# Kernel optimization log

Measured on AMD Instinct MI355X. Metric: run time of the kernel, lower is better.

Reference implementation:

```python
import jax, jax.numpy as jnp
import numpy as np

EPS = 1e-5
GROUPS = 8


def setup_inputs() -> dict:
    key = jax.random.key(0)
    ks = jax.random.split(key, 3)
    b, c, h, w = 8, 256, 64, 64
    x = jax.random.normal(ks[0], (b, c, h, w), dtype=jnp.float32)
    # 1x1 convs are just channel matmuls; store weights as [out_ch, in_ch]
    qkv_w = jax.random.normal(ks[1], (3 * c, c), dtype=jnp.float32) * (c ** -0.5)
    qkv_b = jnp.zeros((3 * c,), dtype=jnp.float32)
    out_w = jax.random.normal(ks[2], (c, c), dtype=jnp.float32) * (c ** -0.5)
    out_b = jnp.zeros((c,), dtype=jnp.float32)
    gn_w = jnp.ones((c,), dtype=jnp.float32)
    gn_b = jnp.zeros((c,), dtype=jnp.float32)
    return {"x": x, "gn_w": gn_w, "gn_b": gn_b, "qkv_w": qkv_w,
            "qkv_b": qkv_b, "out_w": out_w, "out_b": out_b}


def _group_norm(x, gn_w, gn_b):
    # x: [b, c, h, w]; normalize per (group, sample) over (c//g, h, w)
    b, c, h, w = x.shape
    xg = x.reshape(b, GROUPS, c // GROUPS, h * w)
    mean = xg.mean(axis=(2, 3), keepdims=True)
    var = xg.var(axis=(2, 3), keepdims=True)
    xn = (xg - mean) * jax.lax.rsqrt(var + EPS)
    xn = xn.reshape(b, c, h * w)
    return xn * gn_w[None, :, None] + gn_b[None, :, None]


def reference(x, gn_w, gn_b, qkv_w, qkv_b, out_w, out_b):
    b, c, h, w = x.shape
    scale = 1.0 / np.sqrt(c).astype(np.float32)  # matches channels ** -0.5
    nx = _group_norm(x, gn_w, gn_b)                       # [b, c, n]
    qkv = jnp.einsum('oc,bcn->bon', qkv_w, nx) + qkv_b[None, :, None]
    q, k, v = qkv[:, :c], qkv[:, c:2 * c], qkv[:, 2 * c:]  # each [b, c, n]
    attn = jnp.einsum('bci,bcj->bij', q, k) * scale        # [b, n, n]
    attn = jax.nn.softmax(attn, axis=-1)
    out = jnp.einsum('bij,bcj->bci', attn, v)              # [b, c, n]
    out = jnp.einsum('oc,bcn->bon', out_w, out) + out_b[None, :, None]
    return out.reshape(b, c, h, w) + x
```

## Files before the change

### kernel.cpp

```cpp
#include <hip/hip_runtime.h>
#include <math.h>


#define Bn 8
#define Cn 256
#define HWn 4096
#define Gn 8
#define CPGn 32
#define Mqkv 768
#define EPSf 1e-5f
#define QSCALEf 0.0625f
#define RTHR 8.0f

typedef short bf16x8 __attribute__((ext_vector_type(8)));
typedef float f32x4 __attribute__((ext_vector_type(4)));

__device__ __forceinline__ unsigned short f2bf(float f) {
  union { float f; unsigned u; } v; v.f = f;
  unsigned r = v.u + 0x7FFFu + ((v.u >> 16) & 1u);
  return (unsigned short)(r >> 16);
}

__device__ __forceinline__ int cvt_pk_bf16(float lo, float hi) {
  int d;
  asm("v_cvt_pk_bf16_f32 %0, %1, %2" : "=v"(d) : "v"(lo), "v"(hi));
  return d;
}

__global__ __launch_bounds__(1024)
void gn_stats_kernel(const float* __restrict__ x, const float* __restrict__ gn_w,
                     const float* __restrict__ gn_b, float* __restrict__ s_out,
                     float* __restrict__ t_out) {
  const int b = blockIdx.x / Gn, g = blockIdx.x % Gn;
  const float4* base = (const float4*)(x + ((size_t)(b * Cn + g * CPGn)) * HWn);
  const int n4 = CPGn * HWn / 4;
  float sum = 0.f, sq = 0.f;
  for (int i = threadIdx.x; i < n4; i += 1024) {
    float4 v = base[i];
    sum += (v.x + v.y) + (v.z + v.w);
    sq  += (v.x * v.x + v.y * v.y) + (v.z * v.z + v.w * v.w);
  }
  __shared__ float ss[1024], s2[1024];
  ss[threadIdx.x] = sum; s2[threadIdx.x] = sq;
  __syncthreads();
  for (int off = 512; off > 0; off >>= 1) {
    if ((int)threadIdx.x < off) {
      ss[threadIdx.x] += ss[threadIdx.x + off];
      s2[threadIdx.x] += s2[threadIdx.x + off];
    }
    __syncthreads();
  }
  if (threadIdx.x < CPGn) {
    const float inv_n = 1.f / (float)(CPGn * HWn);
    float mean = ss[0] * inv_n;
    float var  = s2[0] * inv_n - mean * mean;
    float rstd = rsqrtf(var + EPSf);
    int c = g * CPGn + (int)threadIdx.x;
    float sc = gn_w[c] * rstd;
    s_out[b * Cn + c] = sc;
    t_out[b * Cn + c] = gn_b[c] - mean * sc;
  }
}

__global__ __launch_bounds__(256)
void affine_transpose_kernel(const float* __restrict__ x, const float* __restrict__ s_aff,
                             const float* __restrict__ t_aff, unsigned short* __restrict__ nxT) {
  const int bid = blockIdx.x;
  const int b = bid & 7, r = bid >> 3;
  const int c0 = (r & 3) * 64, n0 = (r >> 2) * 64;
  const int tid = threadIdx.x;
  __shared__ unsigned int ld32[64][33];
  const float* xb = x + ((size_t)(b * Cn + c0)) * HWn + n0;
  const int cl0 = tid >> 4, nn = (tid & 15) * 4;
#pragma unroll
  for (int it = 0; it < 4; ++it) {
    int cl = cl0 + 16 * it;
    int c = c0 + cl;
    float sc = s_aff[b * Cn + c], sh = t_aff[b * Cn + c];
    float4 v = *(const float4*)(xb + (size_t)cl * HWn + nn);
    ld32[cl][(nn >> 1) + 0] = (unsigned)cvt_pk_bf16(v.x * sc + sh, v.y * sc + sh);
    ld32[cl][(nn >> 1) + 1] = (unsigned)cvt_pk_bf16(v.z * sc + sh, v.w * sc + sh);
  }
  __syncthreads();
#pragma unroll
  for (int it = 0; it < 2; ++it) {
    int chunk = tid + 256 * it;
    int n = chunk >> 3, cg = chunk & 7;
    union { unsigned short u[8]; bf16x8 v; } o;
#pragma unroll
    for (int k = 0; k < 8; ++k) {
      unsigned w32 = ld32[cg * 8 + k][n >> 1];
      o.u[k] = (unsigned short)((n & 1) ? (w32 >> 16) : (w32 & 0xffffu));
    }
    *(bf16x8*)(nxT + ((size_t)(b * HWn + n0 + n)) * Cn + c0 + cg * 8) = o.v;
  }
}

__global__ __launch_bounds__(256, 2)
void qkv_gemm_kernel(const unsigned short* __restrict__ nxT, const float* __restrict__ w,
                     const float* __restrict__ wb, unsigned short* __restrict__ Qt,
                     unsigned short* __restrict__ Kt, unsigned short* __restrict__ Vb) {
  const int bid = blockIdx.x;
  const int b = bid & 7, r = bid >> 3;
  const int n0 = (r & 63) * 64, m0 = (r >> 6) * 128;
  const int tid = threadIdx.x;
  const int wv = tid >> 6, l = tid & 63;
  const int l15 = l & 15, lq = l >> 4;
  const int ob = m0 + wv * 32;

  bf16x8 wf[2][8];
#pragma unroll
  for (int g = 0; g < 2; ++g) {
    const float* wr = w + (size_t)(ob + g * 16 + l15) * Cn + lq * 8;
#pragma unroll
    for (int kc = 0; kc < 8; ++kc) {
      float4 a = *(const float4*)(wr + kc * 32);
      float4 c4 = *(const float4*)(wr + kc * 32 + 4);
      union { int w4[4]; bf16x8 v; } u;
      u.w4[0] = cvt_pk_bf16(a.x, a.y);  u.w4[1] = cvt_pk_bf16(a.z, a.w);
      u.w4[2] = cvt_pk_bf16(c4.x, c4.y); u.w4[3] = cvt_pk_bf16(c4.z, c4.w);
      wf[g][kc] = u.v;
    }
  }

  const unsigned short* nb = nxT + (size_t)b * HWn * Cn + lq * 8;
  f32x4 acc[2][4];
#pragma unroll
  for (int g = 0; g < 2; ++g)
#pragma unroll
    for (int s = 0; s < 4; ++s) acc[g][s] = (f32x4)(0.f);

  const bool isV = (m0 >= 512);
#pragma unroll
  for (int s = 0; s < 4; ++s) {
    const unsigned short* np = nb + (size_t)(n0 + s * 16 + l15) * Cn;
#pragma unroll
    for (int kc = 0; kc < 8; ++kc) {
      bf16x8 xf = *(const bf16x8*)(np + kc * 32);
      if (!isV) {
        acc[0][s] = __builtin_amdgcn_mfma_f32_16x16x32_bf16(wf[0][kc], xf, acc[0][s], 0, 0, 0);
        acc[1][s] = __builtin_amdgcn_mfma_f32_16x16x32_bf16(wf[1][kc], xf, acc[1][s], 0, 0, 0);
      } else {
        acc[0][s] = __builtin_amdgcn_mfma_f32_16x16x32_bf16(xf, wf[0][kc], acc[0][s], 0, 0, 0);
        acc[1][s] = __builtin_amdgcn_mfma_f32_16x16x32_bf16(xf, wf[1][kc], acc[1][s], 0, 0, 0);
      }
    }
  }

  if (!isV) {
    unsigned short* dst = (m0 < 256) ? Qt : Kt;
    const float scl = (m0 < 256) ? QSCALEf : 1.0f;
#pragma unroll
    for (int g = 0; g < 2; ++g) {
      int cb = ((ob + g * 16) & 255) + lq * 4;
      float b0 = wb[ob + g * 16 + lq * 4 + 0];
      float b1 = wb[ob + g * 16 + lq * 4 + 1];
      float b2 = wb[ob + g * 16 + lq * 4 + 2];
      float b3 = wb[ob + g * 16 + lq * 4 + 3];
#pragma unroll
      for (int s = 0; s < 4; ++s) {
        int n = n0 + s * 16 + l15;
        ushort4 pk;
        pk.x = f2bf((acc[g][s][0] + b0) * scl);
        pk.y = f2bf((acc[g][s][1] + b1) * scl);
        pk.z = f2bf((acc[g][s][2] + b2) * scl);
        pk.w = f2bf((acc[g][s][3] + b3) * scl);
        *(ushort4*)(dst + ((size_t)(b * HWn + n)) * Cn + cb) = pk;
      }
    }
  } else {
#pragma unroll
    for (int g = 0; g < 2; ++g) {
      int o = ob + g * 16 + l15;
      int c = o - 512;
      float bias = wb[o];
#pragma unroll
      for (int s = 0; s < 4; ++s) {
        int n = n0 + s * 16 + lq * 4;
        ushort4 pk;
        pk.x = f2bf(acc[g][s][0] + bias);
        pk.y = f2bf(acc[g][s][1] + bias);
        pk.z = f2bf(acc[g][s][2] + bias);
        pk.w = f2bf(acc[g][s][3] + bias);
        *(ushort4*)(Vb + ((size_t)(b * Cn + c)) * HWn + n) = pk;
      }
    }
  }
}

__global__ __launch_bounds__(256, 2)
void attn_kernel(const unsigned short* __restrict__ Qt,
                 const unsigned short* __restrict__ Kt,
                 const unsigned short* __restrict__ Vb,
                 unsigned short* __restrict__ outp) {
  const int bid = blockIdx.x;
  const int b = bid & 7, i0 = (bid >> 3) * 64;
  const int tid = threadIdx.x;
  const int wv = tid >> 6, l = tid & 63;
  const int l15 = l & 15, lq = l >> 4;

  __shared__ unsigned short Ks[8192];
  __shared__ unsigned short Vs[8192];
  char* KsB = (char*)Ks;
  char* VsB = (char*)Vs;

  const unsigned short* Qb = Qt + ((size_t)b * HWn + i0) * Cn;
  const unsigned short* Kb = Kt + (size_t)b * HWn * Cn;
  const unsigned short* Vg = Vb + (size_t)b * Cn * HWn;

  bf16x8 qf[8];
  {
    const unsigned short* qrow = Qb + (size_t)(wv * 16 + l15) * Cn + lq * 8;
#pragma unroll
    for (int kc = 0; kc < 8; ++kc) qf[kc] = *(const bf16x8*)(qrow + kc * 32);
  }

  const int jk = ((tid >> 6) & 1) * 16 + (tid & 15);
  const int ck = (tid >> 7) * 32 + ((tid >> 4) & 3) * 8;
  const int cv = (tid >> 6) * 16 + (tid & 15);
  const int jv = ((tid >> 4) & 3) * 8;
  const unsigned short* gK = Kb + (size_t)jk * Cn + ck;
  const unsigned short* gV = Vg + (size_t)cv * HWn + jv;

  const int laneA = l15 + ((lq & 1) << 5);
  const int laneB = laneA + 16;
  const int shi = lq >> 1;

  bf16x8 kst[4], vst[4];
#pragma unroll
  for (int q = 0; q < 4; ++q) kst[q] = *(const bf16x8*)(gK + q * 64);
#pragma unroll
  for (int q = 0; q < 4; ++q) vst[q] = *(const bf16x8*)(gV + (size_t)q * 64 * HWn);
  gK += 32 * Cn; gV += 32;

  f32x4 o_acc[16];
#pragma unroll
  for (int cs = 0; cs < 16; ++cs) o_acc[cs] = (f32x4)(0.f);
  float m_i = -INFINITY, l_i = 0.f;

#pragma unroll 1
  for (int t = 0; t < 128; ++t) {
#pragma unroll
    for (int q = 0; q < 4; ++q) *(bf16x8*)(KsB + tid * 16 + q * 4096) = kst[q];
#pragma unroll
    for (int q = 0; q < 4; ++q) *(bf16x8*)(VsB + tid * 16 + q * 4096) = vst[q];
    __syncthreads();
    if (t < 127) {
#pragma unroll
      for (int q = 0; q < 4; ++q) kst[q] = *(const bf16x8*)(gK + q * 64);
#pragma unroll
      for (int q = 0; q < 4; ++q) vst[q] = *(const bf16x8*)(gV + (size_t)q * 64 * HWn);
      gK += 32 * Cn; gV += 32;
    }

    f32x4 s0 = (f32x4)(0.f), s1 = (f32x4)(0.f);
#pragma unroll
    for (int kc = 0; kc < 8; ++kc) {
      bf16x8 kf0 = *(const bf16x8*)(KsB + l * 16 + kc * 2048);
      bf16x8 kf1 = *(const bf16x8*)(KsB + l * 16 + kc * 2048 + 1024);
      s0 = __builtin_amdgcn_mfma_f32_16x16x32_bf16(kf0, qf[kc], s0, 0, 0, 0);
      s1 = __builtin_amdgcn_mfma_f32_16x16x32_bf16(kf1, qf[kc], s1, 0, 0, 0);
    }

    float p[2][4];
#pragma unroll
    for (int u = 0; u < 4; ++u) { p[0][u] = s0[u]; p[1][u] = s1[u]; }
    float rm = fmaxf(fmaxf(fmaxf(p[0][0], p[0][1]), fmaxf(p[0][2], p[0][3])),
                     fmaxf(fmaxf(p[1][0], p[1][1]), fmaxf(p[1][2], p[1][3])));
    rm = fmaxf(rm, __shfl_xor(rm, 16));
    rm = fmaxf(rm, __shfl_xor(rm, 32));
    if (!__all(rm - m_i <= RTHR)) {
      float mn = fmaxf(m_i, rm);
      float alpha = __expf(m_i - mn);
      m_i = mn;
      l_i *= alpha;
      float a0 = __shfl(alpha, 4 * lq + 0);
      float a1 = __shfl(alpha, 4 * lq + 1);
      float a2 = __shfl(alpha, 4 * lq + 2);
      float a3 = __shfl(alpha, 4 * lq + 3);
#pragma unroll
      for (int cs = 0; cs < 16; ++cs) {
        o_acc[cs][0] *= a0; o_acc[cs][1] *= a1;
        o_acc[cs][2] *= a2; o_acc[cs][3] *= a3;
      }
    }
    float rs = 0.f;
#pragma unroll
    for (int s = 0; s < 2; ++s)
#pragma unroll
      for (int u = 0; u < 4; ++u) { float e = __expf(p[s][u] - m_i); p[s][u] = e; rs += e; }
    rs += __shfl_xor(rs, 16);
    rs += __shfl_xor(rs, 32);
    l_i += rs;

    int d00 = cvt_pk_bf16(p[0][0], p[0][1]), d01 = cvt_pk_bf16(p[0][2], p[0][3]);
    int d10 = cvt_pk_bf16(p[1][0], p[1][1]), d11 = cvt_pk_bf16(p[1][2], p[1][3]);
    int A00 = __shfl(d00, laneA), A01 = __shfl(d01, laneA);
    int A10 = __shfl(d10, laneA), A11 = __shfl(d11, laneA);
    int B00 = __shfl(d00, laneB), B01 = __shfl(d01, laneB);
    int B10 = __shfl(d10, laneB), B11 = __shfl(d11, laneB);
    union { int w[4]; bf16x8 v; } pa;
    pa.w[0] = shi ? A10 : A00; pa.w[1] = shi ? A11 : A01;
    pa.w[2] = shi ? B10 : B00; pa.w[3] = shi ? B11 : B01;

#pragma unroll
    for (int cs = 0; cs < 16; ++cs) {
      bf16x8 vf = *(const bf16x8*)(VsB + l * 16 + cs * 1024);
      o_acc[cs] = __builtin_amdgcn_mfma_f32_16x16x32_bf16(pa.v, vf, o_acc[cs], 0, 0, 0);
    }
    __syncthreads();
  }

  float il = 1.f / l_i;
  float i0v = __shfl(il, 4 * lq + 0);
  float i1v = __shfl(il, 4 * lq + 1);
  float i2v = __shfl(il, 4 * lq + 2);
  float i3v = __shfl(il, 4 * lq + 3);
  unsigned short* ob = outp + (size_t)b * HWn * Cn;
  const int ibase = i0 + wv * 16 + lq * 4;
#pragma unroll
  for (int cs = 0; cs < 16; ++cs) {
    int c = cs * 16 + l15;
    ob[(size_t)(ibase + 0) * Cn + c] = f2bf(o_acc[cs][0] * i0v);
    ob[(size_t)(ibase + 1) * Cn + c] = f2bf(o_acc[cs][1] * i1v);
    ob[(size_t)(ibase + 2) * Cn + c] = f2bf(o_acc[cs][2] * i2v);
    ob[(size_t)(ibase + 3) * Cn + c] = f2bf(o_acc[cs][3] * i3v);
  }
}

__global__ __launch_bounds__(256, 2)
void out_gemm_kernel(const unsigned short* __restrict__ tmpT, const float* __restrict__ w,
                     const float* __restrict__ wb, const float* __restrict__ xres,
                     float* __restrict__ y) {
  const int bid = blockIdx.x;
  const int b = bid & 7, r = bid >> 3;
  const int n0 = (r & 63) * 64, m0 = (r >> 6) * 128;
  const int tid = threadIdx.x;
  const int wv = tid >> 6, l = tid & 63;
  const int l15 = l & 15, lq = l >> 4;
  const int ob = m0 + wv * 32;

  bf16x8 wf[2][8];
#pragma unroll
  for (int g = 0; g < 2; ++g) {
    const float* wr = w + (size_t)(ob + g * 16 + l15) * Cn + lq * 8;
#pragma unroll
    for (int kc = 0; kc < 8; ++kc) {
      float4 a = *(const float4*)(wr + kc * 32);
      float4 c4 = *(const float4*)(wr + kc * 32 + 4);
      union { int w4[4]; bf16x8 v; } u;
      u.w4[0] = cvt_pk_bf16(a.x, a.y);  u.w4[1] = cvt_pk_bf16(a.z, a.w);
      u.w4[2] = cvt_pk_bf16(c4.x, c4.y); u.w4[3] = cvt_pk_bf16(c4.z, c4.w);
      wf[g][kc] = u.v;
    }
  }

  const unsigned short* tb = tmpT + (size_t)b * HWn * Cn + lq * 8;
  f32x4 acc[2][4];
#pragma unroll
  for (int g = 0; g < 2; ++g)
#pragma unroll
    for (int s = 0; s < 4; ++s) acc[g][s] = (f32x4)(0.f);

#pragma unroll
  for (int s = 0; s < 4; ++s) {
    const unsigned short* tp = tb + (size_t)(n0 + s * 16 + l15) * Cn;
#pragma unroll
    for (int kc = 0; kc < 8; ++kc) {
      bf16x8 tf = *(const bf16x8*)(tp + kc * 32);
      acc[0][s] = __builtin_amdgcn_mfma_f32_16x16x32_bf16(tf, wf[0][kc], acc[0][s], 0, 0, 0);
      acc[1][s] = __builtin_amdgcn_mfma_f32_16x16x32_bf16(tf, wf[1][kc], acc[1][s], 0, 0, 0);
    }
  }

#pragma unroll
  for (int g = 0; g < 2; ++g) {
    int o = ob + g * 16 + l15;
    float bias = wb[o];
#pragma unroll
    for (int s = 0; s < 4; ++s) {
      int n = n0 + s * 16 + lq * 4;
      size_t idx = ((size_t)(b * Cn + o)) * HWn + n;
      float4 xr = *(const float4*)(xres + idx);
      float4 out;
      out.x = acc[g][s][0] + bias + xr.x;
      out.y = acc[g][s][1] + bias + xr.y;
      out.z = acc[g][s][2] + bias + xr.z;
      out.w = acc[g][s][3] + bias + xr.w;
      *(float4*)(y + idx) = out;
    }
  }
}

extern "C" void kernel_launch(void* const* d_in, const int* in_sizes, int n_in,
                              void* d_out, int out_size, void* d_ws, size_t ws_size,
                              hipStream_t stream) {
  (void)in_sizes; (void)n_in; (void)out_size; (void)ws_size;
  const float* x     = (const float*)d_in[0];
  const float* gn_w  = (const float*)d_in[1];
  const float* gn_b  = (const float*)d_in[2];
  const float* qkv_w = (const float*)d_in[3];
  const float* qkv_b = (const float*)d_in[4];
  const float* out_w = (const float*)d_in[5];
  const float* out_b = (const float*)d_in[6];
  float* out = (float*)d_out;

  char* ws = (char*)d_ws;
  float* s_aff = (float*)ws;
  float* t_aff = s_aff + Bn * Cn;
  unsigned short* Qt  = (unsigned short*)(ws + 16384);
  unsigned short* Kt  = Qt  + (size_t)Bn * HWn * Cn;
  unsigned short* Vb  = Kt  + (size_t)Bn * HWn * Cn;
  unsigned short* nxT = Vb  + (size_t)Bn * HWn * Cn;
  unsigned short* tmpT = nxT + (size_t)Bn * HWn * Cn;

  gn_stats_kernel<<<dim3(Bn * Gn), 1024, 0, stream>>>(x, gn_w, gn_b, s_aff, t_aff);
  affine_transpose_kernel<<<dim3(2048), 256, 0, stream>>>(x, s_aff, t_aff, nxT);
  qkv_gemm_kernel<<<dim3(3072), 256, 0, stream>>>(nxT, qkv_w, qkv_b, Qt, Kt, Vb);
  attn_kernel<<<dim3(512), 256, 0, stream>>>(Qt, Kt, Vb, tmpT);
  out_gemm_kernel<<<dim3(1024), 256, 0, stream>>>(tmpT, out_w, out_b, x, out);
}
```

Measured before the change: 397.2 us.

## Split attention over key dimension into four partitions with combine kernel

Splits each attention query tile's key/value range into four partitions, launching four times as many blocks, each writing unnormalized bf16 partial outputs plus running max and sum. A new combine kernel merges the partials with log-sum-exp weights, and the output GEMM reads the combined tile layout. This aims to raise parallelism and improve load balance across CUs, at the cost of extra partial-output memory traffic, an extra launch, and repeated Q loads.

```diff
diff --git a/kernel.cpp b/kernel.cpp
--- a/kernel.cpp
+++ b/kernel.cpp
@@ -19,6 +19,11 @@
   union { float f; unsigned u; } v; v.f = f;
   unsigned r = v.u + 0x7FFFu + ((v.u >> 16) & 1u);
   return (unsigned short)(r >> 16);
+}
+
+__device__ __forceinline__ float bf2f(unsigned short u) {
+  union { unsigned u; float f; } v; v.u = ((unsigned)u) << 16;
+  return v.f;
 }
 
 __device__ __forceinline__ int cvt_pk_bf16(float lo, float hi) {
@@ -192,9 +197,9 @@
 void attn_kernel(const unsigned short* __restrict__ Qt,
                  const unsigned short* __restrict__ Kt,
                  const unsigned short* __restrict__ Vb,
-                 unsigned short* __restrict__ outp) {
+                 unsigned short* __restrict__ pO, float* __restrict__ pML) {
   const int bid = blockIdx.x;
-  const int b = bid & 7, i0 = (bid >> 3) * 64;
+  const int b = bid & 7, part = (bid >> 3) & 3, i0 = (bid >> 5) * 64;
   const int tid = threadIdx.x;
   const int wv = tid >> 6, l = tid & 63;
   const int l15 = l & 15, lq = l >> 4;
@@ -219,8 +224,8 @@
   const int ck = (tid >> 7) * 32 + ((tid >> 4) & 3) * 8;
   const int cv = (tid >> 6) * 16 + (tid & 15);
   const int jv = ((tid >> 4) & 3) * 8;
-  const unsigned short* gK = Kb + (size_t)jk * Cn + ck;
-  const unsigned short* gV = Vg + (size_t)cv * HWn + jv;
+  const unsigned short* gK = Kb + (size_t)(jk + part * 1024) * Cn + ck;
+  const unsigned short* gV = Vg + (size_t)cv * HWn + jv + part * 1024;
 
   const int laneA = l15 + ((lq & 1) << 5);
   const int laneB = laneA + 16;
@@ -239,13 +244,13 @@
   float m_i = -INFINITY, l_i = 0.f;
 
 #pragma unroll 1
-  for (int t = 0; t < 128; ++t) {
+  for (int t = 0; t < 32; ++t) {
 #pragma unroll
     for (int q = 0; q < 4; ++q) *(bf16x8*)(KsB + tid * 16 + q * 4096) = kst[q];
 #pragma unroll
     for (int q = 0; q < 4; ++q) *(bf16x8*)(VsB + tid * 16 + q * 4096) = vst[q];
     __syncthreads();
-    if (t < 127) {
+    if (t < 31) {
 #pragma unroll
       for (int q = 0; q < 4; ++q) kst[q] = *(const bf16x8*)(gK + q * 64);
 #pragma unroll
@@ -311,25 +316,72 @@
     __syncthreads();
   }
 
-  float il = 1.f / l_i;
-  float i0v = __shfl(il, 4 * lq + 0);
-  float i1v = __shfl(il, 4 * lq + 1);
-  float i2v = __shfl(il, 4 * lq + 2);
-  float i3v = __shfl(il, 4 * lq + 3);
-  unsigned short* ob = outp + (size_t)b * HWn * Cn;
-  const int ibase = i0 + wv * 16 + lq * 4;
+  unsigned short* pOb = pO + (size_t)bid * (64 * 256);
+  const int ibase = wv * 16 + lq * 4;
 #pragma unroll
   for (int cs = 0; cs < 16; ++cs) {
     int c = cs * 16 + l15;
-    ob[(size_t)(ibase + 0) * Cn + c] = f2bf(o_acc[cs][0] * i0v);
-    ob[(size_t)(ibase + 1) * Cn + c] = f2bf(o_acc[cs][1] * i1v);
-    ob[(size_t)(ibase + 2) * Cn + c] = f2bf(o_acc[cs][2] * i2v);
-    ob[(size_t)(ibase + 3) * Cn + c] = f2bf(o_acc[cs][3] * i3v);
+    pOb[(ibase + 0) * 256 + c] = f2bf(o_acc[cs][0]);
+    pOb[(ibase + 1) * 256 + c] = f2bf(o_acc[cs][1]);
+    pOb[(ibase + 2) * 256 + c] = f2bf(o_acc[cs][2]);
+    pOb[(ibase + 3) * 256 + c] = f2bf(o_acc[cs][3]);
+  }
+  if (lq == 0) {
+    pML[(size_t)bid * 128 + (wv * 16 + l15) * 2 + 0] = m_i;
+    pML[(size_t)bid * 128 + (wv * 16 + l15) * 2 + 1] = l_i;
+  }
+}
+
+__global__ __launch_bounds__(256)
+void attn_combine_kernel(unsigned short* __restrict__ pO, const float* __restrict__ pML) {
+  const int bid = blockIdx.x;
+  const int b = bid & 7, itile = bid >> 3;
+  const int tid = threadIdx.x;
+  const int p0id = b + (itile << 5);
+  unsigned short* B0 = pO + (size_t)p0id * (64 * 256);
+  const unsigned short* B1 = pO + (size_t)(p0id + 8)  * (64 * 256);
+  const unsigned short* B2 = pO + (size_t)(p0id + 16) * (64 * 256);
+  const unsigned short* B3 = pO + (size_t)(p0id + 24) * (64 * 256);
+
+  __shared__ float gS[4][64];
+  if (tid < 64) {
+    float m0v = pML[(size_t)p0id * 128 + tid * 2],        l0v = pML[(size_t)p0id * 128 + tid * 2 + 1];
+    float m1v = pML[(size_t)(p0id + 8) * 128 + tid * 2],  l1v = pML[(size_t)(p0id + 8) * 128 + tid * 2 + 1];
+    float m2v = pML[(size_t)(p0id + 16) * 128 + tid * 2], l2v = pML[(size_t)(p0id + 16) * 128 + tid * 2 + 1];
+    float m3v = pML[(size_t)(p0id + 24) * 128 + tid * 2], l3v = pML[(size_t)(p0id + 24) * 128 + tid * 2 + 1];
+    float ms = fmaxf(fmaxf(m0v, m1v), fmaxf(m2v, m3v));
+    float w0 = __expf(m0v - ms), w1 = __expf(m1v - ms);
+    float w2 = __expf(m2v - ms), w3 = __expf(m3v - ms);
+    float den = w0 * l0v + w1 * l1v + w2 * l2v + w3 * l3v;
+    float id = 1.f / den;
+    gS[0][tid] = w0 * id; gS[1][tid] = w1 * id;
+    gS[2][tid] = w2 * id; gS[3][tid] = w3 * id;
+  }
+  __syncthreads();
+
+#pragma unroll
+  for (int k = 0; k < 8; ++k) {
+    int chunk = tid + 256 * k;
+    int row = chunk >> 5, cc = (chunk & 31) * 8;
+    int off = row * 256 + cc;
+    float g0 = gS[0][row], g1 = gS[1][row], g2 = gS[2][row], g3 = gS[3][row];
+    union { unsigned short u[8]; bf16x8 v; } v0, v1, v2, v3, o;
+    v0.v = *(const bf16x8*)(B0 + off);
+    v1.v = *(const bf16x8*)(B1 + off);
+    v2.v = *(const bf16x8*)(B2 + off);
+    v3.v = *(const bf16x8*)(B3 + off);
+#pragma unroll
+    for (int e = 0; e < 8; ++e) {
+      float val = g0 * bf2f(v0.u[e]) + g1 * bf2f(v1.u[e]) +
+                  g2 * bf2f(v2.u[e]) + g3 * bf2f(v3.u[e]);
+      o.u[e] = f2bf(val);
+    }
+    *(bf16x8*)(B0 + off) = o.v;
   }
 }
 
 __global__ __launch_bounds__(256, 2)
-void out_gemm_kernel(const unsigned short* __restrict__ tmpT, const float* __restrict__ w,
+void out_gemm_kernel(const unsigned short* __restrict__ pO, const float* __restrict__ w,
                      const float* __restrict__ wb, const float* __restrict__ xres,
                      float* __restrict__ y) {
   const int bid = blockIdx.x;
@@ -355,7 +407,7 @@
     }
   }
 
-  const unsigned short* tb = tmpT + (size_t)b * HWn * Cn + lq * 8;
+  const unsigned short* tb = pO + ((size_t)(b + ((n0 >> 6) << 5)) * (64 * 256)) + lq * 8;
   f32x4 acc[2][4];
 #pragma unroll
   for (int g = 0; g < 2; ++g)
@@ -364,7 +416,7 @@
 
 #pragma unroll
   for (int s = 0; s < 4; ++s) {
-    const unsigned short* tp = tb + (size_t)(n0 + s * 16 + l15) * Cn;
+    const unsigned short* tp = tb + (size_t)(s * 16 + l15) * Cn;
 #pragma unroll
     for (int kc = 0; kc < 8; ++kc) {
       bf16x8 tf = *(const bf16x8*)(tp + kc * 32);
@@ -406,17 +458,20 @@
   float* out = (float*)d_out;
 
   char* ws = (char*)d_ws;
+  const size_t BHC = (size_t)Bn * HWn * Cn;
   float* s_aff = (float*)ws;
   float* t_aff = s_aff + Bn * Cn;
   unsigned short* Qt  = (unsigned short*)(ws + 16384);
-  unsigned short* Kt  = Qt  + (size_t)Bn * HWn * Cn;
-  unsigned short* Vb  = Kt  + (size_t)Bn * HWn * Cn;
-  unsigned short* nxT = Vb  + (size_t)Bn * HWn * Cn;
-  unsigned short* tmpT = nxT + (size_t)Bn * HWn * Cn;
+  unsigned short* Kt  = Qt + BHC;
+  unsigned short* Vb  = Kt + BHC;
+  unsigned short* nxT = Vb + BHC;
+  unsigned short* pO  = nxT;
+  float* pML = (float*)((char*)pO + (size_t)2048 * 16384 * 2);
 
   gn_stats_kernel<<<dim3(Bn * Gn), 1024, 0, stream>>>(x, gn_w, gn_b, s_aff, t_aff);
   affine_transpose_kernel<<<dim3(2048), 256, 0, stream>>>(x, s_aff, t_aff, nxT);
   qkv_gemm_kernel<<<dim3(3072), 256, 0, stream>>>(nxT, qkv_w, qkv_b, Qt, Kt, Vb);
-  attn_kernel<<<dim3(512), 256, 0, stream>>>(Qt, Kt, Vb, tmpT);
-  out_gemm_kernel<<<dim3(1024), 256, 0, stream>>>(tmpT, out_w, out_b, x, out);
-}
+  attn_kernel<<<dim3(2048), 256, 0, stream>>>(Qt, Kt, Vb, pO, pML);
+  attn_combine_kernel<<<dim3(512), 256, 0, stream>>>(pO, pML);
+  out_gemm_kernel<<<dim3(1024), 256, 0, stream>>>(pO, out_w, out_b, x, out);
+}
```

Result: slower. 424.5 us (+6.9%).

## Switch attention kernel to 32x32x16 MFMA with split query/channel wave tiling

Applied to the files above, without the earlier changes.

The flash-attention kernel moves from 16x16x32 to 32x32x16 bf16 MFMA. Waves now tile as 2 query groups of 32 rows by 2 channel halves, where before each of the 4 waves owned 16 query rows. The K/V staging layouts and the P fragment exchange change to match: a single xor-32 shuffle replaces the laneA/laneB gathers, and the per-row alpha and 1/l broadcast shuffles go away. Final stores become vectorized ushort4 writes. The aim is fewer LDS reads per FLOP and less shuffle overhead. In exchange, the QK^T product is computed twice, once per channel-half wave, which adds redundant MFMA work.

```diff
diff --git a/kernel.cpp b/kernel.cpp
--- a/kernel.cpp
+++ b/kernel.cpp
@@ -14,6 +14,7 @@
 
 typedef short bf16x8 __attribute__((ext_vector_type(8)));
 typedef float f32x4 __attribute__((ext_vector_type(4)));
+typedef float f32x16 __attribute__((ext_vector_type(16)));
 
 __device__ __forceinline__ unsigned short f2bf(float f) {
   union { float f; unsigned u; } v; v.f = f;
@@ -197,7 +198,8 @@
   const int b = bid & 7, i0 = (bid >> 3) * 64;
   const int tid = threadIdx.x;
   const int wv = tid >> 6, l = tid & 63;
-  const int l15 = l & 15, lq = l >> 4;
+  const int l31 = l & 31, hi = l >> 5;
+  const int rg = wv >> 1, cw = wv & 1;
 
   __shared__ unsigned short Ks[8192];
   __shared__ unsigned short Vs[8192];
@@ -208,23 +210,16 @@
   const unsigned short* Kb = Kt + (size_t)b * HWn * Cn;
   const unsigned short* Vg = Vb + (size_t)b * Cn * HWn;
 
-  bf16x8 qf[8];
+  bf16x8 qf[16];
   {
-    const unsigned short* qrow = Qb + (size_t)(wv * 16 + l15) * Cn + lq * 8;
-#pragma unroll
-    for (int kc = 0; kc < 8; ++kc) qf[kc] = *(const bf16x8*)(qrow + kc * 32);
-  }
-
-  const int jk = ((tid >> 6) & 1) * 16 + (tid & 15);
-  const int ck = (tid >> 7) * 32 + ((tid >> 4) & 3) * 8;
-  const int cv = (tid >> 6) * 16 + (tid & 15);
-  const int jv = ((tid >> 4) & 3) * 8;
-  const unsigned short* gK = Kb + (size_t)jk * Cn + ck;
-  const unsigned short* gV = Vg + (size_t)cv * HWn + jv;
-
-  const int laneA = l15 + ((lq & 1) << 5);
-  const int laneB = laneA + 16;
-  const int shi = lq >> 1;
+    const unsigned short* qrow = Qb + (size_t)(rg * 32 + l31) * Cn + hi * 8;
+#pragma unroll
+    for (int kc = 0; kc < 16; ++kc) qf[kc] = *(const bf16x8*)(qrow + kc * 16);
+  }
+
+  const unsigned short* gK = Kb + (size_t)(tid & 31) * Cn + (tid >> 5) * 8;
+  const unsigned short* gV = Vg + (size_t)((tid >> 7) * 32 + (tid & 31)) * HWn
+                                + ((tid >> 5) & 3) * 8;
 
   bf16x8 kst[4], vst[4];
 #pragma unroll
@@ -233,10 +228,10 @@
   for (int q = 0; q < 4; ++q) vst[q] = *(const bf16x8*)(gV + (size_t)q * 64 * HWn);
   gK += 32 * Cn; gV += 32;
 
-  f32x4 o_acc[16];
-#pragma unroll
-  for (int cs = 0; cs < 16; ++cs) o_acc[cs] = (f32x4)(0.f);
+  f32x16 o0 = (f32x16)(0.f), o1 = (f32x16)(0.f);
+  f32x16 o2 = (f32x16)(0.f), o3 = (f32x16)(0.f);
   float m_i = -INFINITY, l_i = 0.f;
+  const int vbase = cw * 4 * 2048;
 
 #pragma unroll 1
   for (int t = 0; t < 128; ++t) {
@@ -253,78 +248,89 @@
       gK += 32 * Cn; gV += 32;
     }
 
-    f32x4 s0 = (f32x4)(0.f), s1 = (f32x4)(0.f);
-#pragma unroll
-    for (int kc = 0; kc < 8; ++kc) {
-      bf16x8 kf0 = *(const bf16x8*)(KsB + l * 16 + kc * 2048);
-      bf16x8 kf1 = *(const bf16x8*)(KsB + l * 16 + kc * 2048 + 1024);
-      s0 = __builtin_amdgcn_mfma_f32_16x16x32_bf16(kf0, qf[kc], s0, 0, 0, 0);
-      s1 = __builtin_amdgcn_mfma_f32_16x16x32_bf16(kf1, qf[kc], s1, 0, 0, 0);
-    }
-
-    float p[2][4];
-#pragma unroll
-    for (int u = 0; u < 4; ++u) { p[0][u] = s0[u]; p[1][u] = s1[u]; }
-    float rm = fmaxf(fmaxf(fmaxf(p[0][0], p[0][1]), fmaxf(p[0][2], p[0][3])),
-                     fmaxf(fmaxf(p[1][0], p[1][1]), fmaxf(p[1][2], p[1][3])));
-    rm = fmaxf(rm, __shfl_xor(rm, 16));
+    f32x16 sa = (f32x16)(0.f);
+#pragma unroll
+    for (int kc = 0; kc < 16; ++kc) {
+      bf16x8 kf = *(const bf16x8*)(KsB + l * 16 + kc * 1024);
+      sa = __builtin_amdgcn_mfma_f32_32x32x16_bf16(kf, qf[kc], sa, 0, 0, 0);
+    }
+
+    float p[16];
+#pragma unroll
+    for (int r = 0; r < 16; ++r) p[r] = sa[r];
+    float rm = p[0];
+#pragma unroll
+    for (int r = 1; r < 16; ++r) rm = fmaxf(rm, p[r]);
     rm = fmaxf(rm, __shfl_xor(rm, 32));
     if (!__all(rm - m_i <= RTHR)) {
       float mn = fmaxf(m_i, rm);
       float alpha = __expf(m_i - mn);
       m_i = mn;
       l_i *= alpha;
-      float a0 = __shfl(alpha, 4 * lq + 0);
-      float a1 = __shfl(alpha, 4 * lq + 1);
-      float a2 = __shfl(alpha, 4 * lq + 2);
-      float a3 = __shfl(alpha, 4 * lq + 3);
-#pragma unroll
-      for (int cs = 0; cs < 16; ++cs) {
-        o_acc[cs][0] *= a0; o_acc[cs][1] *= a1;
-        o_acc[cs][2] *= a2; o_acc[cs][3] *= a3;
+#pragma unroll
+      for (int r = 0; r < 16; ++r) {
+        o0[r] *= alpha; o1[r] *= alpha; o2[r] *= alpha; o3[r] *= alpha;
       }
     }
     float rs = 0.f;
 #pragma unroll
-    for (int s = 0; s < 2; ++s)
-#pragma unroll
-      for (int u = 0; u < 4; ++u) { float e = __expf(p[s][u] - m_i); p[s][u] = e; rs += e; }
-    rs += __shfl_xor(rs, 16);
+    for (int r = 0; r < 16; ++r) { p[r] = __expf(p[r] - m_i); rs += p[r]; }
     rs += __shfl_xor(rs, 32);
     l_i += rs;
 
-    int d00 = cvt_pk_bf16(p[0][0], p[0][1]), d01 = cvt_pk_bf16(p[0][2], p[0][3]);
-    int d10 = cvt_pk_bf16(p[1][0], p[1][1]), d11 = cvt_pk_bf16(p[1][2], p[1][3]);
-    int A00 = __shfl(d00, laneA), A01 = __shfl(d01, laneA);
-    int A10 = __shfl(d10, laneA), A11 = __shfl(d11, laneA);
-    int B00 = __shfl(d00, laneB), B01 = __shfl(d01, laneB);
-    int B10 = __shfl(d10, laneB), B11 = __shfl(d11, laneB);
-    union { int w[4]; bf16x8 v; } pa;
-    pa.w[0] = shi ? A10 : A00; pa.w[1] = shi ? A11 : A01;
-    pa.w[2] = shi ? B10 : B00; pa.w[3] = shi ? B11 : B01;
-
-#pragma unroll
-    for (int cs = 0; cs < 16; ++cs) {
-      bf16x8 vf = *(const bf16x8*)(VsB + l * 16 + cs * 1024);
-      o_acc[cs] = __builtin_amdgcn_mfma_f32_16x16x32_bf16(pa.v, vf, o_acc[cs], 0, 0, 0);
+    int d0 = cvt_pk_bf16(p[0],  p[1]),  d1 = cvt_pk_bf16(p[2],  p[3]);
+    int d2 = cvt_pk_bf16(p[4],  p[5]),  d3 = cvt_pk_bf16(p[6],  p[7]);
+    int d4 = cvt_pk_bf16(p[8],  p[9]),  d5 = cvt_pk_bf16(p[10], p[11]);
+    int d6 = cvt_pk_bf16(p[12], p[13]), d7 = cvt_pk_bf16(p[14], p[15]);
+    int x0 = __shfl_xor(d0, 32), x1 = __shfl_xor(d1, 32);
+    int x2 = __shfl_xor(d2, 32), x3 = __shfl_xor(d3, 32);
+    int x4 = __shfl_xor(d4, 32), x5 = __shfl_xor(d5, 32);
+    int x6 = __shfl_xor(d6, 32), x7 = __shfl_xor(d7, 32);
+    union { int w[4]; bf16x8 v; } pf0, pf1;
+    pf0.w[0] = hi ? x2 : d0; pf0.w[1] = hi ? x3 : d1;
+    pf0.w[2] = hi ? d2 : x0; pf0.w[3] = hi ? d3 : x1;
+    pf1.w[0] = hi ? x6 : d4; pf1.w[1] = hi ? x7 : d5;
+    pf1.w[2] = hi ? d6 : x4; pf1.w[3] = hi ? d7 : x5;
+
+    {
+      bf16x8 vf0 = *(const bf16x8*)(VsB + l * 16 + vbase + 0 * 2048);
+      bf16x8 vf1 = *(const bf16x8*)(VsB + l * 16 + vbase + 0 * 2048 + 1024);
+      o0 = __builtin_amdgcn_mfma_f32_32x32x16_bf16(vf0, pf0.v, o0, 0, 0, 0);
+      o0 = __builtin_amdgcn_mfma_f32_32x32x16_bf16(vf1, pf1.v, o0, 0, 0, 0);
+      vf0 = *(const bf16x8*)(VsB + l * 16 + vbase + 1 * 2048);
+      vf1 = *(const bf16x8*)(VsB + l * 16 + vbase + 1 * 2048 + 1024);
+      o1 = __builtin_amdgcn_mfma_f32_32x32x16_bf16(vf0, pf0.v, o1, 0, 0, 0);
+      o1 = __builtin_amdgcn_mfma_f32_32x32x16_bf16(vf1, pf1.v, o1, 0, 0, 0);
+      vf0 = *(const bf16x8*)(VsB + l * 16 + vbase + 2 * 2048);
+      vf1 = *(const bf16x8*)(VsB + l * 16 + vbase + 2 * 2048 + 1024);
+      o2 = __builtin_amdgcn_mfma_f32_32x32x16_bf16(vf0, pf0.v, o2, 0, 0, 0);
+      o2 = __builtin_amdgcn_mfma_f32_32x32x16_bf16(vf1, pf1.v, o2, 0, 0, 0);
+      vf0 = *(const bf16x8*)(VsB + l * 16 + vbase + 3 * 2048);
+      vf1 = *(const bf16x8*)(VsB + l * 16 + vbase + 3 * 2048 + 1024);
+      o3 = __builtin_amdgcn_mfma_f32_32x32x16_bf16(vf0, pf0.v, o3, 0, 0, 0);
+      o3 = __builtin_amdgcn_mfma_f32_32x32x16_bf16(vf1, pf1.v, o3, 0, 0, 0);
     }
     __syncthreads();
   }
 
   float il = 1.f / l_i;
-  float i0v = __shfl(il, 4 * lq + 0);
-  float i1v = __shfl(il, 4 * lq + 1);
-  float i2v = __shfl(il, 4 * lq + 2);
-  float i3v = __shfl(il, 4 * lq + 3);
-  unsigned short* ob = outp + (size_t)b * HWn * Cn;
-  const int ibase = i0 + wv * 16 + lq * 4;
-#pragma unroll
-  for (int cs = 0; cs < 16; ++cs) {
-    int c = cs * 16 + l15;
-    ob[(size_t)(ibase + 0) * Cn + c] = f2bf(o_acc[cs][0] * i0v);
-    ob[(size_t)(ibase + 1) * Cn + c] = f2bf(o_acc[cs][1] * i1v);
-    ob[(size_t)(ibase + 2) * Cn + c] = f2bf(o_acc[cs][2] * i2v);
-    ob[(size_t)(ibase + 3) * Cn + c] = f2bf(o_acc[cs][3] * i3v);
+  unsigned short* ob = outp + ((size_t)b * HWn + (size_t)(i0 + rg * 32 + l31)) * Cn;
+  const int cb0 = cw * 128 + 4 * hi;
+#pragma unroll
+  for (int rq = 0; rq < 4; ++rq) {
+    ushort4 s0v, s1v, s2v, s3v;
+    s0v.x = f2bf(o0[rq * 4 + 0] * il); s0v.y = f2bf(o0[rq * 4 + 1] * il);
+    s0v.z = f2bf(o0[rq * 4 + 2] * il); s0v.w = f2bf(o0[rq * 4 + 3] * il);
+    s1v.x = f2bf(o1[rq * 4 + 0] * il); s1v.y = f2bf(o1[rq * 4 + 1] * il);
+    s1v.z = f2bf(o1[rq * 4 + 2] * il); s1v.w = f2bf(o1[rq * 4 + 3] * il);
+    s2v.x = f2bf(o2[rq * 4 + 0] * il); s2v.y = f2bf(o2[rq * 4 + 1] * il);
+    s2v.z = f2bf(o2[rq * 4 + 2] * il); s2v.w = f2bf(o2[rq * 4 + 3] * il);
+    s3v.x = f2bf(o3[rq * 4 + 0] * il); s3v.y = f2bf(o3[rq * 4 + 1] * il);
+    s3v.z = f2bf(o3[rq * 4 + 2] * il); s3v.w = f2bf(o3[rq * 4 + 3] * il);
+    *(ushort4*)(ob + cb0 + 0 * 32 + 8 * rq) = s0v;
+    *(ushort4*)(ob + cb0 + 1 * 32 + 8 * rq) = s1v;
+    *(ushort4*)(ob + cb0 + 2 * 32 + 8 * rq) = s2v;
+    *(ushort4*)(ob + cb0 + 3 * 32 + 8 * rq) = s3v;
   }
 }
 
```

New measurement: 420.1 us. 1.06x slower.
